# Kernel tuning notes

Measured on AMD Instinct MI355X. Metric: run time of the kernel, lower is better.

The kernel has to match this reference:

```python
import jax, jax.numpy as jnp
import numpy as np

B, S, D, H = 4, 2048, 1024, 16
HD = D // H


def setup_inputs() -> dict:
    key = jax.random.key(0)
    ks = jax.random.split(key, 11)
    s = 1.0 / np.sqrt(D)
    inp = {
        "query": jax.random.normal(ks[0], (B, S, D), jnp.float32),
        "key": jax.random.normal(ks[1], (B, S, D), jnp.float32),
        "value": jax.random.normal(ks[2], (B, S, D), jnp.float32),
        "Wq": jax.random.normal(ks[3], (D, D), jnp.float32) * s,
        "bq": jnp.zeros((D,), jnp.float32),
        "Wk": jax.random.normal(ks[4], (D, D), jnp.float32) * s,
        "bk": jnp.zeros((D,), jnp.float32),
        "Wv": jax.random.normal(ks[5], (D, D), jnp.float32) * s,
        "bv": jnp.zeros((D,), jnp.float32),
        "Wo": jax.random.normal(ks[6], (D, D), jnp.float32) * s,
        "bo": jnp.zeros((D,), jnp.float32),
    }
    return inp


def reference(query, key, value, Wq, bq, Wk, bk, Wv, bv, Wo, bo):
    scale = 1.0 / np.sqrt(HD).astype(np.float32)
    # Linear projections (torch Linear: x @ W.T + b), split into heads -> [B,H,S,HD]
    def proj(x, W, b):
        y = x @ W.T + b
        return y.reshape(B, S, H, HD).transpose(0, 2, 1, 3)

    q = proj(query, Wq, bq)
    k = proj(key, Wk, bk)
    v = proj(value, Wv, bv)
    scores = jnp.einsum("bhqd,bhkd->bhqk", q, k) * scale  # [B,H,S,S]
    weights = jax.nn.softmax(scores, axis=-1)
    attn = jnp.einsum("bhqk,bhkd->bhqd", weights, v)
    attn = attn.transpose(0, 2, 1, 3).reshape(B, S, D)
    return attn @ Wo.T + bo
```

## Files before the change

### kernel.cpp

```cpp
#include <hip/hip_runtime.h>
#include <hip/hip_bf16.h>
#include <stdint.h>

#define Bn 4
#define Sn 2048
#define Dn 1024
#define Hn 16
#define HDn 64
#define Mn (Bn * Sn)
#define PS 44

typedef __attribute__((ext_vector_type(8))) __bf16 bf16x8;
typedef __attribute__((ext_vector_type(4))) __bf16 bf16x4;
typedef __attribute__((ext_vector_type(4))) float f32x4;

#if __has_builtin(__builtin_amdgcn_exp2f)
#define EXP2F(x) __builtin_amdgcn_exp2f(x)
#else
#define EXP2F(x) exp2f(x)
#endif

typedef __attribute__((address_space(1))) unsigned int as1_uint;
typedef __attribute__((address_space(3))) unsigned int as3_uint;

__device__ __forceinline__ void gld_lds16(const void* g, void* l) {
  __builtin_amdgcn_global_load_lds((const as1_uint*)g, (as3_uint*)l, 16, 0, 0);
}

struct CvtArgs {
  const float* src[7];
};
__constant__ const size_t kGb[8] = {0,       1048576, 2097152, 3145728,
                                    3276800, 3407872, 3538944, 3670016};

__global__ __launch_bounds__(256) void cvt_all(CvtArgs a, __bf16* __restrict__ dst) {
  size_t i = (size_t)blockIdx.x * 256 + threadIdx.x;
  if (i >= 3670016) return;
  int s = 0;
#pragma unroll
  for (int k = 1; k < 7; k++) s += (i >= kGb[k]) ? 1 : 0;
  const float4* sp = (const float4*)a.src[s] + 2 * (i - kGb[s]);
  float4 x = sp[0], y = sp[1];
  bf16x8 o;
  o[0] = (__bf16)x.x; o[1] = (__bf16)x.y; o[2] = (__bf16)x.z; o[3] = (__bf16)x.w;
  o[4] = (__bf16)y.x; o[5] = (__bf16)y.y; o[6] = (__bf16)y.z; o[7] = (__bf16)y.w;
  *(bf16x8*)(dst + 8 * i) = o;
}

template <int MODE>
__device__ __forceinline__ void gemm128_body(const __bf16* __restrict__ A,
                                             const __bf16* __restrict__ Bw,
                                             const float* __restrict__ bias,
                                             void* __restrict__ Cout, int m0, int n0,
                                             float scale) {
  __shared__ __align__(16) __bf16 lA[128 * 32];
  __shared__ __align__(16) __bf16 lB[128 * 32];
  const int tid = threadIdx.x;
  const int wave = tid >> 6, lane = tid & 63, quad = lane >> 4, l15 = lane & 15;
  const int wm = wave >> 1, wn = wave & 1;
  f32x4 acc[4][4] = {};
  const char* Ab = (const char*)(A + (size_t)m0 * Dn);
  const char* Bb = (const char*)(Bw + (size_t)n0 * Dn);
  char* lAc = (char*)lA;
  char* lBc = (char*)lB;
  const int o0 = tid * 16, o1 = o0 + 4096;
  const int r0 = o0 >> 6, c0 = o0 & 63;
  const int r1 = o1 >> 6, c1 = o1 & 63;

  for (int k0 = 0; k0 < Dn; k0 += 32) {
    __syncthreads();
    gld_lds16(Ab + (size_t)r0 * 2048 + k0 * 2 + c0, lAc + o0);
    gld_lds16(Ab + (size_t)r1 * 2048 + k0 * 2 + c1, lAc + o1);
    gld_lds16(Bb + (size_t)r0 * 2048 + k0 * 2 + c0, lBc + o0);
    gld_lds16(Bb + (size_t)r1 * 2048 + k0 * 2 + c1, lBc + o1);
    __syncthreads();
    bf16x8 af[4], bfv[4];
#pragma unroll
    for (int i = 0; i < 4; i++)
      af[i] = *(const bf16x8*)(lA + (wm * 64 + i * 16 + l15) * 32 + quad * 8);
#pragma unroll
    for (int t = 0; t < 4; t++)
      bfv[t] = *(const bf16x8*)(lB + (wn * 64 + t * 16 + l15) * 32 + quad * 8);
#pragma unroll
    for (int i = 0; i < 4; i++)
#pragma unroll
      for (int t = 0; t < 4; t++)
        acc[i][t] = __builtin_amdgcn_mfma_f32_16x16x32_bf16(af[i], bfv[t], acc[i][t], 0, 0, 0);
  }
#pragma unroll
  for (int i = 0; i < 4; i++) {
    const int rowb = m0 + wm * 64 + i * 16 + quad * 4;
#pragma unroll
    for (int t = 0; t < 4; t++) {
      const int col = n0 + wn * 64 + t * 16 + l15;
      const float bb = bias[col];
      if (MODE == 2) {
        const int b = rowb >> 11, s = rowb & 2047;
        const int h = col >> 6, c = col & 63;
        bf16x4 pk;
#pragma unroll
        for (int r = 0; r < 4; r++) pk[r] = (__bf16)(acc[i][t][r] + bb);
        *(bf16x4*)((__bf16*)Cout + (((size_t)(b * Hn + h) * HDn + c) * Sn + s)) = pk;
      } else {
#pragma unroll
        for (int r = 0; r < 4; r++) {
          float v = (acc[i][t][r] + bb) * scale;
          if (MODE == 1)
            ((float*)Cout)[(size_t)(rowb + r) * Dn + col] = v;
          else
            ((__bf16*)Cout)[(size_t)(rowb + r) * Dn + col] = (__bf16)v;
        }
      }
    }
  }
}

__global__ __launch_bounds__(256, 3) void qkv_gemm(
    const __bf16* __restrict__ X, const __bf16* __restrict__ W,
    const float* __restrict__ bq, const float* __restrict__ bk,
    const float* __restrict__ bv, __bf16* __restrict__ out) {
  const int lin = blockIdx.x + (blockIdx.y << 3) + (blockIdx.z << 9);
  const int wg = (lin & 7) * 192 + (lin >> 3);
  const int z = wg >> 9, rem = wg & 511;
  const int m0 = (rem >> 3) * 128, n0 = (rem & 7) * 128;
  if (z == 0) {
    gemm128_body<0>(X, W, bq, out, m0, n0, 0.18033688011112042f);
  } else if (z == 1) {
    gemm128_body<0>(X + (size_t)Mn * Dn, W + (size_t)Dn * Dn, bk,
                    out + (size_t)Mn * Dn, m0, n0, 1.0f);
  } else {
    gemm128_body<2>(X + 2 * (size_t)Mn * Dn, W + 2 * (size_t)Dn * Dn, bv,
                    out + 2 * (size_t)Mn * Dn, m0, n0, 1.0f);
  }
}

__global__ __launch_bounds__(256, 3) void out_gemm(const __bf16* __restrict__ A,
                                                   const __bf16* __restrict__ W,
                                                   const float* __restrict__ bo,
                                                   float* __restrict__ out) {
  const int lin = blockIdx.x + (blockIdx.y << 3);
  const int wg = (lin & 7) * 64 + (lin >> 3);
  const int m0 = (wg >> 3) * 128, n0 = (wg & 7) * 128;
  gemm128_body<1>(A, W, bo, out, m0, n0, 1.0f);
}

__global__ __launch_bounds__(256, 2) void flash_attn(const __bf16* __restrict__ Q,
                                                     const __bf16* __restrict__ K,
                                                     const __bf16* __restrict__ Vt,
                                                     __bf16* __restrict__ Aout) {
  __shared__ __align__(16) __bf16 plds[4][64 * PS];
  const int tid = threadIdx.x;
  const int wave = tid >> 6, lane = tid & 63, quad = lane >> 4, l15 = lane & 15;
  const int lin = blockIdx.x + (blockIdx.y << 3);
  const int wg = (lin & 7) * 64 + (lin >> 3);
  const int bh = wg >> 3, qt = wg & 7;
  const int b = bh >> 4, h = bh & 15;
  const int q0 = qt * 256 + wave * 64;
  const __bf16* Qb = Q + ((size_t)b * Sn) * Dn + h * HDn;
  const __bf16* Kb = K + ((size_t)b * Sn) * Dn + h * HDn;
  const __bf16* Vtb = Vt + (size_t)(b * Hn + h) * HDn * Sn;
  __bf16* myP = &plds[wave][0];

  bf16x8 qf[4][2];
#pragma unroll
  for (int iq = 0; iq < 4; iq++)
#pragma unroll
    for (int s = 0; s < 2; s++)
      qf[iq][s] = *(const bf16x8*)(Qb + (size_t)(q0 + iq * 16 + l15) * Dn + s * 32 + quad * 8);

  f32x4 O[4][4] = {};
  float li[4] = {};

  bf16x8 kf[2][2][2];
  bf16x8 vf[2][4];
#pragma unroll
  for (int tk = 0; tk < 2; tk++)
#pragma unroll
    for (int s = 0; s < 2; s++)
      kf[0][tk][s] = *(const bf16x8*)(Kb + (size_t)(tk * 16 + l15) * Dn + s * 32 + quad * 8);
#pragma unroll
  for (int mc = 0; mc < 4; mc++)
    vf[0][mc] = *(const bf16x8*)(Vtb + (size_t)(mc * 16 + l15) * Sn + quad * 8);

#pragma unroll 2
  for (int kt = 0; kt < Sn / 32; kt++) {
    const int cur = kt & 1, nxt = cur ^ 1;
    f32x4 sa[2][4];
    __builtin_amdgcn_s_setprio(1);
#pragma unroll
    for (int tk = 0; tk < 2; tk++)
#pragma unroll
      for (int iq = 0; iq < 4; iq++) {
        f32x4 z = {0.f, 0.f, 0.f, 0.f};
        z = __builtin_amdgcn_mfma_f32_16x16x32_bf16(kf[cur][tk][0], qf[iq][0], z, 0, 0, 0);
        z = __builtin_amdgcn_mfma_f32_16x16x32_bf16(kf[cur][tk][1], qf[iq][1], z, 0, 0, 0);
        sa[tk][iq] = z;
      }
    __builtin_amdgcn_s_setprio(0);
    if (kt < Sn / 32 - 1) {
      const int key0 = (kt + 1) * 32;
#pragma unroll
      for (int tk = 0; tk < 2; tk++)
#pragma unroll
        for (int s = 0; s < 2; s++)
          kf[nxt][tk][s] =
              *(const bf16x8*)(Kb + (size_t)(key0 + tk * 16 + l15) * Dn + s * 32 + quad * 8);
#pragma unroll
      for (int mc = 0; mc < 4; mc++)
        vf[nxt][mc] = *(const bf16x8*)(Vtb + (size_t)(mc * 16 + l15) * Sn + key0 + quad * 8);
    }
#pragma unroll
    for (int tk = 0; tk < 2; tk++)
#pragma unroll
      for (int iq = 0; iq < 4; iq++) {
        bf16x4 pk;
#pragma unroll
        for (int r = 0; r < 4; r++) {
          float p = EXP2F(sa[tk][iq][r]);
          li[iq] += p;
          pk[r] = (__bf16)p;
        }
        *(bf16x4*)(myP + (iq * 16 + l15) * PS + tk * 16 + quad * 4) = pk;
      }
    __builtin_amdgcn_s_setprio(1);
#pragma unroll
    for (int iq = 0; iq < 4; iq++) {
      bf16x4 plo = *(const bf16x4*)(myP + (iq * 16 + l15) * PS + quad * 8);
      bf16x4 phi = *(const bf16x4*)(myP + (iq * 16 + l15) * PS + quad * 8 + 4);
      bf16x8 pf = __builtin_shufflevector(plo, phi, 0, 1, 2, 3, 4, 5, 6, 7);
#pragma unroll
      for (int mc = 0; mc < 4; mc++)
        O[mc][iq] = __builtin_amdgcn_mfma_f32_16x16x32_bf16(vf[cur][mc], pf, O[mc][iq], 0, 0, 0);
    }
    __builtin_amdgcn_s_setprio(0);
  }
  float inv[4];
#pragma unroll
  for (int iq = 0; iq < 4; iq++) {
    float s = li[iq];
    s += __shfl_xor(s, 16);
    s += __shfl_xor(s, 32);
    inv[iq] = 1.0f / s;
  }
#pragma unroll
  for (int mc = 0; mc < 4; mc++)
#pragma unroll
    for (int iq = 0; iq < 4; iq++) {
      bf16x4 o;
#pragma unroll
      for (int r = 0; r < 4; r++) o[r] = (__bf16)(O[mc][iq][r] * inv[iq]);
      *(bf16x4*)(Aout + ((size_t)b * Sn + q0 + iq * 16 + l15) * Dn + h * HDn + mc * 16 +
                 quad * 4) = o;
    }
}

extern "C" void kernel_launch(void* const* d_in, const int* in_sizes, int n_in,
                              void* d_out, int out_size, void* d_ws, size_t ws_size,
                              hipStream_t stream) {
  const float* bq = (const float*)d_in[4];
  const float* bk = (const float*)d_in[6];
  const float* bv = (const float*)d_in[8];
  const float* bo = (const float*)d_in[10];

  const size_t MD = (size_t)Mn * Dn;
  const size_t DD = (size_t)Dn * Dn;
  __bf16* Xbf  = (__bf16*)d_ws;
  __bf16* Wbf  = Xbf + 3 * MD;
  __bf16* QKV  = Wbf + 4 * DD;
  __bf16* Attn = QKV + 3 * MD;

  CvtArgs ca;
  ca.src[0] = (const float*)d_in[0];
  ca.src[1] = (const float*)d_in[1];
  ca.src[2] = (const float*)d_in[2];
  ca.src[3] = (const float*)d_in[3];
  ca.src[4] = (const float*)d_in[5];
  ca.src[5] = (const float*)d_in[7];
  ca.src[6] = (const float*)d_in[9];
  cvt_all<<<14336, 256, 0, stream>>>(ca, Xbf);

  qkv_gemm<<<dim3(Dn / 128, Mn / 128, 3), 256, 0, stream>>>(Xbf, Wbf, bq, bk, bv, QKV);
  flash_attn<<<dim3(Sn / 256, Bn * Hn), 256, 0, stream>>>(QKV, QKV + MD, QKV + 2 * MD, Attn);
  out_gemm<<<dim3(Dn / 128, Mn / 128), 256, 0, stream>>>(Attn, Wbf + 3 * DD, bo, (float*)d_out);
}
```

Baseline: 383.6 us.

## Stage K/V tiles in LDS via global-to-LDS loads shared across waves

In flash attention, each wave used to load its own K and V fragments from global memory into registers. Now the whole workgroup cooperatively copies each 32-key K tile and V tile into double-buffered, XOR-swizzled LDS with direct global-to-LDS loads, and every wave reads its fragments from there. This removes the 4x redundant global traffic across the four waves. In exchange it adds a workgroup barrier every iteration, extra LDS space that may reduce occupancy, and LDS read latency before the MFMAs.

```diff
diff --git a/kernel.cpp b/kernel.cpp
--- a/kernel.cpp
+++ b/kernel.cpp
@@ -149,6 +149,8 @@
                                                      const __bf16* __restrict__ Vt,
                                                      __bf16* __restrict__ Aout) {
   __shared__ __align__(16) __bf16 plds[4][64 * PS];
+  __shared__ __align__(16) __bf16 kbuf[2][32 * 64];
+  __shared__ __align__(16) __bf16 vbuf[2][32 * 64];
   const int tid = threadIdx.x;
   const int wave = tid >> 6, lane = tid & 63, quad = lane >> 4, l15 = lane & 15;
   const int lin = blockIdx.x + (blockIdx.y << 3);
@@ -157,9 +159,24 @@
   const int b = bh >> 4, h = bh & 15;
   const int q0 = qt * 256 + wave * 64;
   const __bf16* Qb = Q + ((size_t)b * Sn) * Dn + h * HDn;
-  const __bf16* Kb = K + ((size_t)b * Sn) * Dn + h * HDn;
-  const __bf16* Vtb = Vt + (size_t)(b * Hn + h) * HDn * Sn;
+  const char* Kbase = (const char*)(K + ((size_t)b * Sn) * Dn + h * HDn);
+  const char* Vbase = (const char*)(Vt + (size_t)(b * Hn + h) * HDn * Sn);
   __bf16* myP = &plds[wave][0];
+
+  const int srow = tid >> 3;
+  const int kjsrc = (tid & 7) ^ (srow & 7);
+  const int vjsrc = (tid & 7) ^ (srow & 7);
+  const int vhalf = vjsrc >> 2, vsq = vjsrc & 3;
+  const size_t ksrc_row = (size_t)srow * (Dn * 2) + kjsrc * 16;
+  const size_t vsrc_row = (size_t)(srow + 32 * vhalf) * (Sn * 2) + vsq * 16;
+
+#define STAGE(BUFI, KEY0)                                                         \
+  {                                                                               \
+    gld_lds16(Kbase + (size_t)(KEY0) * (Dn * 2) + ksrc_row,                       \
+              (char*)&kbuf[BUFI][0] + tid * 16);                                  \
+    gld_lds16(Vbase + (size_t)(KEY0) * 2 + vsrc_row,                              \
+              (char*)&vbuf[BUFI][0] + tid * 16);                                  \
+  }
 
   bf16x8 qf[4][2];
 #pragma unroll
@@ -171,20 +188,28 @@
   f32x4 O[4][4] = {};
   float li[4] = {};
 
-  bf16x8 kf[2][2][2];
-  bf16x8 vf[2][4];
-#pragma unroll
-  for (int tk = 0; tk < 2; tk++)
-#pragma unroll
-    for (int s = 0; s < 2; s++)
-      kf[0][tk][s] = *(const bf16x8*)(Kb + (size_t)(tk * 16 + l15) * Dn + s * 32 + quad * 8);
-#pragma unroll
-  for (int mc = 0; mc < 4; mc++)
-    vf[0][mc] = *(const bf16x8*)(Vtb + (size_t)(mc * 16 + l15) * Sn + quad * 8);
+  STAGE(0, 0)
+  __syncthreads();
 
 #pragma unroll 2
   for (int kt = 0; kt < Sn / 32; kt++) {
     const int cur = kt & 1, nxt = cur ^ 1;
+    if (kt < Sn / 32 - 1) STAGE(nxt, (kt + 1) * 32)
+    bf16x8 kf[2][2], vf[4];
+#pragma unroll
+    for (int tk = 0; tk < 2; tk++)
+#pragma unroll
+      for (int s = 0; s < 2; s++) {
+        const int jp = (s * 4 + quad) ^ (l15 & 7);
+        kf[tk][s] = *(const bf16x8*)((const char*)&kbuf[cur][0] +
+                                     (tk * 16 + l15) * 128 + jp * 16);
+      }
+#pragma unroll
+    for (int mc = 0; mc < 4; mc++) {
+      const int jp = ((mc >> 1) * 4 + quad) ^ (l15 & 7);
+      vf[mc] = *(const bf16x8*)((const char*)&vbuf[cur][0] +
+                                ((mc & 1) * 16 + l15) * 128 + jp * 16);
+    }
     f32x4 sa[2][4];
     __builtin_amdgcn_s_setprio(1);
 #pragma unroll
@@ -192,23 +217,11 @@
 #pragma unroll
       for (int iq = 0; iq < 4; iq++) {
         f32x4 z = {0.f, 0.f, 0.f, 0.f};
-        z = __builtin_amdgcn_mfma_f32_16x16x32_bf16(kf[cur][tk][0], qf[iq][0], z, 0, 0, 0);
-        z = __builtin_amdgcn_mfma_f32_16x16x32_bf16(kf[cur][tk][1], qf[iq][1], z, 0, 0, 0);
+        z = __builtin_amdgcn_mfma_f32_16x16x32_bf16(kf[tk][0], qf[iq][0], z, 0, 0, 0);
+        z = __builtin_amdgcn_mfma_f32_16x16x32_bf16(kf[tk][1], qf[iq][1], z, 0, 0, 0);
         sa[tk][iq] = z;
       }
     __builtin_amdgcn_s_setprio(0);
-    if (kt < Sn / 32 - 1) {
-      const int key0 = (kt + 1) * 32;
-#pragma unroll
-      for (int tk = 0; tk < 2; tk++)
-#pragma unroll
-        for (int s = 0; s < 2; s++)
-          kf[nxt][tk][s] =
-              *(const bf16x8*)(Kb + (size_t)(key0 + tk * 16 + l15) * Dn + s * 32 + quad * 8);
-#pragma unroll
-      for (int mc = 0; mc < 4; mc++)
-        vf[nxt][mc] = *(const bf16x8*)(Vtb + (size_t)(mc * 16 + l15) * Sn + key0 + quad * 8);
-    }
 #pragma unroll
     for (int tk = 0; tk < 2; tk++)
 #pragma unroll
@@ -230,10 +243,12 @@
       bf16x8 pf = __builtin_shufflevector(plo, phi, 0, 1, 2, 3, 4, 5, 6, 7);
 #pragma unroll
       for (int mc = 0; mc < 4; mc++)
-        O[mc][iq] = __builtin_amdgcn_mfma_f32_16x16x32_bf16(vf[cur][mc], pf, O[mc][iq], 0, 0, 0);
+        O[mc][iq] = __builtin_amdgcn_mfma_f32_16x16x32_bf16(vf[mc], pf, O[mc][iq], 0, 0, 0);
     }
     __builtin_amdgcn_s_setprio(0);
-  }
+    __syncthreads();
+  }
+#undef STAGE
   float inv[4];
 #pragma unroll
   for (int iq = 0; iq < 4; iq++) {
```

After: 329.9 us. 1.16x faster.
